# Performance work log

Hardware: AMD Instinct MI355X
Metric: run time of the kernel (lower is better)

The kernel has to match this reference:

```python
import jax, jax.numpy as jnp
import numpy as np

B, T, C, H = 8, 2048, 2048, 128  # batch, seq, n_embd, head_size


def setup_inputs() -> dict:
    key = jax.random.key(0)
    kx, kq, kk, kv = jax.random.split(key, 4)
    x = jax.random.normal(kx, (B, T, C), dtype=jnp.float32)
    # Linear(n_embd, head_size, bias=False); stored as [in, out] so x @ W matches x @ weight.T in torch
    Wq = jax.random.normal(kq, (C, H), dtype=jnp.float32) * 0.02
    Wk = jax.random.normal(kk, (C, H), dtype=jnp.float32) * 0.02
    Wv = jax.random.normal(kv, (C, H), dtype=jnp.float32) * 0.02
    return {"x": x, "Wq": Wq, "Wk": Wk, "Wv": Wv}


def reference(x, Wq, Wk, Wv):
    # Single-head scaled dot-product attention (mask=False path of the module)
    q = jnp.einsum("btc,ch->bth", x, Wq)  # [B,T,H]
    k = jnp.einsum("btc,ch->bth", x, Wk)
    v = jnp.einsum("btc,ch->bth", x, Wv)
    scale = k.shape[-1] ** -0.5
    wei = jnp.einsum("bqh,bkh->bqk", q, k) * scale  # [B,T,T]
    wei = jax.nn.softmax(wei, axis=-1)
    out = jnp.einsum("bqk,bkh->bqh", wei, v)  # [B,T,H]
    return out
```

## Files before the change

### kernel.cpp

```cpp
#include <hip/hip_runtime.h>
#include <hip/hip_bf16.h>

typedef __attribute__((ext_vector_type(8))) short short8;
typedef __attribute__((ext_vector_type(4))) float f32x4;

#define MFMA16(a, b, c) __builtin_amdgcn_mfma_f32_16x16x32_bf16((a), (b), (c), 0, 0, 0)

#define GLOAD_LDS16(gp, lp)                                                            \
    __builtin_amdgcn_global_load_lds(                                                  \
        (const __attribute__((address_space(1))) unsigned int*)(gp),                   \
        (__attribute__((address_space(3))) unsigned int*)(lp), 16, 0, 0)

__device__ __forceinline__ unsigned short f2bf(float f) {
    __hip_bfloat16 h = __float2bfloat16(f);
    return __builtin_bit_cast(unsigned short, h);
}

__device__ __forceinline__ short8 cvt8(f32x4 a, f32x4 b) {
    short8 r;
    r[0] = (short)f2bf(a[0]); r[1] = (short)f2bf(a[1]);
    r[2] = (short)f2bf(a[2]); r[3] = (short)f2bf(a[3]);
    r[4] = (short)f2bf(b[0]); r[5] = (short)f2bf(b[1]);
    r[6] = (short)f2bf(b[2]); r[7] = (short)f2bf(b[3]);
    return r;
}

__global__ __launch_bounds__(256) void wt_kernel(const float* __restrict__ Wq,
                                                 const float* __restrict__ Wk,
                                                 const float* __restrict__ Wv,
                                                 unsigned short* __restrict__ Wt) {
    __shared__ float T[64][65];
    const int j = blockIdx.z;
    const float* W = (j == 0) ? Wq : (j == 1) ? Wk : Wv;
    const int c0 = blockIdx.x * 64;
    const int h0 = blockIdx.y * 64;
    const int tid = threadIdx.x;

#pragma unroll
    for (int i = 0; i < 4; i++) {
        const int cc = tid + 256 * i;
        const int r = cc >> 4;
        const int q4 = (cc & 15) * 4;
        f32x4 vv = *(const f32x4*)(W + (size_t)(c0 + r) * 128 + h0 + q4);
        T[r][q4 + 0] = vv[0]; T[r][q4 + 1] = vv[1];
        T[r][q4 + 2] = vv[2]; T[r][q4 + 3] = vv[3];
    }
    __syncthreads();
#pragma unroll
    for (int i = 0; i < 2; i++) {
        const int oc = tid + 256 * i;
        const int hr = oc >> 3;
        const int c8 = (oc & 7) * 8;
        short8 r;
#pragma unroll
        for (int e = 0; e < 8; e++) r[e] = (short)f2bf(T[c8 + e][hr]);
        *(short8*)(Wt + (size_t)j * (128 * 2048) + (size_t)(h0 + hr) * 2048 + c0 + c8) = r;
    }
}

__global__ __launch_bounds__(256, 3) void qkv_gemm(const float* __restrict__ x,
                                                   const unsigned short* __restrict__ Wt,
                                                   unsigned short* __restrict__ qkv) {
    constexpr int LDA = 72;
    __shared__ __align__(16) unsigned short As[2][64 * LDA];
    __shared__ __align__(16) unsigned short Bs[2][128 * 64];

    const int tid = threadIdx.x;
    const int l = tid & 63;
    const int w = tid >> 6;
    const int wr = w >> 1, wc = w & 1;
    const int lrow = l & 15, g = l >> 4, lk = g * 8;

    const int p = blockIdx.x;
    const int wg = (p & 7) * 96 + (p >> 3);
    const int bn = wg % 3;
    const int bm = wg / 3;

    const float* xA = x + (size_t)bm * 64 * 2048;
    const unsigned short* Wb = Wt + (size_t)bn * (128 * 2048);
    unsigned short* outp = qkv + (size_t)bn * (16384 * 128);

    const int rowA = tid >> 2;
    const int quad = tid & 3;
    const float* srcA0 = xA + (size_t)rowA * 2048 + quad * 16;

    const int brow_base = (w << 5) + (l >> 3);
    const int bsw = ((l >> 3) & 7) << 4;
    const int bslot = (l & 7) << 4;
    const int bsrc_off = ((bslot ^ bsw) >> 1);

    const f32x4 fzero = {0.f, 0.f, 0.f, 0.f};
    f32x4 acc[2][4];
#pragma unroll
    for (int mt = 0; mt < 2; mt++)
#pragma unroll
        for (int nt = 0; nt < 4; nt++) acc[mt][nt] = fzero;

#pragma unroll
    for (int i = 0; i < 4; i++) {
        const int row = brow_base + (i << 3);
        GLOAD_LDS16(Wb + (size_t)row * 2048 + bsrc_off,
                    &Bs[0][(w << 11) + (i << 9)]);
    }
    {
        f32x4 a0 = *(const f32x4*)(srcA0);
        f32x4 a1 = *(const f32x4*)(srcA0 + 4);
        f32x4 a2 = *(const f32x4*)(srcA0 + 8);
        f32x4 a3 = *(const f32x4*)(srcA0 + 12);
        *(short8*)&As[0][rowA * LDA + quad * 16] = cvt8(a0, a1);
        *(short8*)&As[0][rowA * LDA + quad * 16 + 8] = cvt8(a2, a3);
    }
    __syncthreads();

    int cur = 0;
    for (int kt = 0; kt < 32; kt++) {
        f32x4 a0, a1, a2, a3;
        if (kt < 31) {
#pragma unroll
            for (int i = 0; i < 4; i++) {
                const int row = brow_base + (i << 3);
                GLOAD_LDS16(Wb + (size_t)row * 2048 + (kt + 1) * 64 + bsrc_off,
                            &Bs[cur ^ 1][(w << 11) + (i << 9)]);
            }
            const float* sA = srcA0 + (kt + 1) * 64;
            a0 = *(const f32x4*)(sA);
            a1 = *(const f32x4*)(sA + 4);
            a2 = *(const f32x4*)(sA + 8);
            a3 = *(const f32x4*)(sA + 12);
        }

#pragma unroll
        for (int ks = 0; ks < 2; ks++) {
            short8 af[2], bfr[4];
#pragma unroll
            for (int mt = 0; mt < 2; mt++)
                af[mt] = *(const short8*)&As[cur][(wr * 32 + mt * 16 + lrow) * LDA + ks * 32 + lk];
#pragma unroll
            for (int nt = 0; nt < 4; nt++) {
                const int n = wc * 64 + nt * 16 + lrow;
                const int kbyte = (ks * 64 + g * 16) ^ ((n & 7) << 4);
                bfr[nt] = *(const short8*)&Bs[cur][n * 64 + (kbyte >> 1)];
            }
#pragma unroll
            for (int mt = 0; mt < 2; mt++)
#pragma unroll
                for (int nt = 0; nt < 4; nt++)
                    acc[mt][nt] = MFMA16(af[mt], bfr[nt], acc[mt][nt]);
        }

        if (kt < 31) {
            *(short8*)&As[cur ^ 1][rowA * LDA + quad * 16] = cvt8(a0, a1);
            *(short8*)&As[cur ^ 1][rowA * LDA + quad * 16 + 8] = cvt8(a2, a3);
        }
        __syncthreads();
        cur ^= 1;
    }

    const float scale = (bn == 0) ? 0.08838834764831845f : 1.0f;
#pragma unroll
    for (int mt = 0; mt < 2; mt++)
#pragma unroll
        for (int nt = 0; nt < 4; nt++)
#pragma unroll
            for (int r = 0; r < 4; r++) {
                const int row = bm * 64 + wr * 32 + mt * 16 + g * 4 + r;
                const int col = wc * 64 + nt * 16 + lrow;
                outp[(size_t)row * 128 + col] = f2bf(acc[mt][nt][r] * scale);
            }
}

template <bool SPLIT>
__global__ __launch_bounds__(256) void attn_kernel_t(const unsigned short* __restrict__ q,
                                                     const unsigned short* __restrict__ k,
                                                     const unsigned short* __restrict__ v,
                                                     float* __restrict__ Oout,
                                                     float* __restrict__ Ml) {
    constexpr int KS = 136;
    constexpr int VS = 88;
    constexpr int PS = 88;
    __shared__ __align__(16) unsigned short Ks[64 * KS];
    __shared__ __align__(16) unsigned short Vt[128 * VS];
    __shared__ __align__(16) unsigned short Psh[64 * PS];

    const int tid = threadIdx.x;
    const int l = tid & 63;
    const int w = tid >> 6;
    const int qt = blockIdx.x;
    const int b = blockIdx.y;
    const int s = SPLIT ? blockIdx.z : 0;
    const int kv_beg = SPLIT ? s * 11 : 0;
    const int kv_end = SPLIT ? ((s == 2) ? 32 : kv_beg + 11) : 32;
    const int lrow = l & 15, g = l >> 4, lk = g * 8;

    const size_t qbase = ((size_t)b * 2048 + qt * 64 + w * 16 + lrow) * 128;
    short8 qf[4];
#pragma unroll
    for (int ks = 0; ks < 4; ks++) qf[ks] = *(const short8*)(q + qbase + ks * 32 + lk);

    const f32x4 fzero = {0.f, 0.f, 0.f, 0.f};
    float m_r[4], l_r[4];
    f32x4 oacc[8];
#pragma unroll
    for (int r = 0; r < 4; r++) { m_r[r] = -1e30f; l_r[r] = 0.f; }
#pragma unroll
    for (int d = 0; d < 8; d++) oacc[d] = fzero;

    const int skey = tid & 63;
    const int sd = (tid >> 6) * 8;

    for (int kv = kv_beg; kv < kv_end; kv++) {
        __syncthreads();
        const size_t kvbase = ((size_t)b * 2048 + kv * 64 + skey) * 128;
#pragma unroll
        for (int jj = 0; jj < 4; jj++) {
            const int d0 = sd + jj * 32;
            short8 kvv = *(const short8*)(k + kvbase + d0);
            *(short8*)&Ks[skey * KS + d0] = kvv;
        }
#pragma unroll
        for (int jj = 0; jj < 4; jj++) {
            const int d0 = sd + jj * 32;
            short8 vv = *(const short8*)(v + kvbase + d0);
#pragma unroll
            for (int e = 0; e < 8; e++)
                Vt[(d0 + e) * VS + skey] = (unsigned short)vv[e];
        }
        __syncthreads();

        f32x4 sv[4];
#pragma unroll
        for (int nt = 0; nt < 4; nt++) sv[nt] = fzero;
#pragma unroll
        for (int ks = 0; ks < 4; ks++)
#pragma unroll
            for (int nt = 0; nt < 4; nt++) {
                short8 kf = *(const short8*)&Ks[(nt * 16 + lrow) * KS + ks * 32 + lk];
                sv[nt] = MFMA16(qf[ks], kf, sv[nt]);
            }

        float sf[4];
#pragma unroll
        for (int r = 0; r < 4; r++) {
            float tmax = fmaxf(fmaxf(sv[0][r], sv[1][r]), fmaxf(sv[2][r], sv[3][r]));
#pragma unroll
            for (int mk = 8; mk >= 1; mk >>= 1) tmax = fmaxf(tmax, __shfl_xor(tmax, mk));
            const float mnew = fmaxf(m_r[r], tmax);
            sf[r] = __expf(m_r[r] - mnew);
            m_r[r] = mnew;
            float psum = 0.f;
#pragma unroll
            for (int nt = 0; nt < 4; nt++) {
                const float pp = __expf(sv[nt][r] - mnew);
                sv[nt][r] = pp;
                psum += pp;
            }
#pragma unroll
            for (int mk = 8; mk >= 1; mk >>= 1) psum += __shfl_xor(psum, mk);
            l_r[r] = l_r[r] * sf[r] + psum;
        }
#pragma unroll
        for (int d = 0; d < 8; d++)
#pragma unroll
            for (int r = 0; r < 4; r++) oacc[d][r] *= sf[r];

#pragma unroll
        for (int nt = 0; nt < 4; nt++)
#pragma unroll
            for (int r = 0; r < 4; r++)
                Psh[(w * 16 + g * 4 + r) * PS + nt * 16 + lrow] = f2bf(sv[nt][r]);
        __syncthreads();

#pragma unroll
        for (int ks2 = 0; ks2 < 2; ks2++) {
            short8 pa = *(const short8*)&Psh[(w * 16 + lrow) * PS + ks2 * 32 + lk];
#pragma unroll
            for (int dt = 0; dt < 8; dt++) {
                short8 vbf = *(const short8*)&Vt[(dt * 16 + lrow) * VS + ks2 * 32 + lk];
                oacc[dt] = MFMA16(pa, vbf, oacc[dt]);
            }
        }
    }

#pragma unroll
    for (int r = 0; r < 4; r++) {
        const int rowi = b * 2048 + qt * 64 + w * 16 + g * 4 + r;
        if (SPLIT) {
            const size_t obase = ((size_t)s * 16384 + rowi) * 128;
#pragma unroll
            for (int dt = 0; dt < 8; dt++)
                Oout[obase + dt * 16 + lrow] = oacc[dt][r];
            if (lrow == 0) {
                const size_t mb = ((size_t)s * 16384 + rowi) * 2;
                Ml[mb] = m_r[r];
                Ml[mb + 1] = l_r[r];
            }
        } else {
            const float inv = 1.0f / l_r[r];
#pragma unroll
            for (int dt = 0; dt < 8; dt++)
                Oout[(size_t)rowi * 128 + dt * 16 + lrow] = oacc[dt][r] * inv;
        }
    }
}

__global__ __launch_bounds__(256) void attn_merge(const float* __restrict__ Oacc,
                                                  const float* __restrict__ Ml,
                                                  float* __restrict__ out) {
    const int row = blockIdx.x * 2 + (threadIdx.x >> 7);
    const int c = threadIdx.x & 127;
    const float m0 = Ml[(size_t)(0 * 16384 + row) * 2], l0 = Ml[(size_t)(0 * 16384 + row) * 2 + 1];
    const float m1 = Ml[(size_t)(1 * 16384 + row) * 2], l1 = Ml[(size_t)(1 * 16384 + row) * 2 + 1];
    const float m2 = Ml[(size_t)(2 * 16384 + row) * 2], l2 = Ml[(size_t)(2 * 16384 + row) * 2 + 1];
    const float M = fmaxf(m0, fmaxf(m1, m2));
    const float w0 = __expf(m0 - M), w1 = __expf(m1 - M), w2 = __expf(m2 - M);
    const float D = w0 * l0 + w1 * l1 + w2 * l2;
    const float o = w0 * Oacc[(size_t)(0 * 16384 + row) * 128 + c] +
                    w1 * Oacc[(size_t)(1 * 16384 + row) * 128 + c] +
                    w2 * Oacc[(size_t)(2 * 16384 + row) * 128 + c];
    out[(size_t)row * 128 + c] = o / D;
}

extern "C" void kernel_launch(void* const* d_in, const int* in_sizes, int n_in,
                              void* d_out, int out_size, void* d_ws, size_t ws_size,
                              hipStream_t stream) {
    const float* x  = (const float*)d_in[0];
    const float* Wq = (const float*)d_in[1];
    const float* Wk = (const float*)d_in[2];
    const float* Wv = (const float*)d_in[3];
    float* out = (float*)d_out;

    unsigned short* ws = (unsigned short*)d_ws;
    unsigned short* qb = ws;
    unsigned short* kb = qb + (size_t)16384 * 128;
    unsigned short* vb = kb + (size_t)16384 * 128;
    unsigned short* Wt = vb + (size_t)16384 * 128;
    float* Oacc = (float*)(Wt + (size_t)3 * 128 * 2048);
    float* Ml = Oacc + (size_t)3 * 16384 * 128;
    const size_t ws_need = (size_t)((char*)(Ml + (size_t)3 * 16384 * 2) - (char*)d_ws);

    hipLaunchKernelGGL(wt_kernel, dim3(32, 2, 3), dim3(256), 0, stream, Wq, Wk, Wv, Wt);
    hipLaunchKernelGGL(qkv_gemm, dim3(768), dim3(256), 0, stream, x, Wt, qb);
    if (ws_size >= ws_need) {
        hipLaunchKernelGGL((attn_kernel_t<true>), dim3(32, 8, 3), dim3(256), 0, stream,
                           qb, kb, vb, Oacc, Ml);
        hipLaunchKernelGGL(attn_merge, dim3(8192), dim3(256), 0, stream, Oacc, Ml, out);
    } else {
        hipLaunchKernelGGL((attn_kernel_t<false>), dim3(32, 8), dim3(256), 0, stream,
                           qb, kb, vb, out, (float*)nullptr);
    }
}
```

Measured before the change: 293.0 us.

## Deepen QKV GEMM prefetch and pre-transpose V for register-prefetched split attention

```diff
diff --git a/kernel.cpp b/kernel.cpp
--- a/kernel.cpp
+++ b/kernel.cpp
@@ -61,8 +61,7 @@
 __global__ __launch_bounds__(256, 3) void qkv_gemm(const float* __restrict__ x,
                                                    const unsigned short* __restrict__ Wt,
                                                    unsigned short* __restrict__ qkv) {
-    constexpr int LDA = 72;
-    __shared__ __align__(16) unsigned short As[2][64 * LDA];
+    __shared__ __align__(16) unsigned short As[2][64 * 72];
     __shared__ __align__(16) unsigned short Bs[2][128 * 64];
 
     const int tid = threadIdx.x;
@@ -96,65 +95,88 @@
 #pragma unroll
         for (int nt = 0; nt < 4; nt++) acc[mt][nt] = fzero;
 
-#pragma unroll
-    for (int i = 0; i < 4; i++) {
-        const int row = brow_base + (i << 3);
-        GLOAD_LDS16(Wb + (size_t)row * 2048 + bsrc_off,
-                    &Bs[0][(w << 11) + (i << 9)]);
-    }
+    f32x4 pA[4], pB[4];
+
+#define QKV_COMPUTE(CUR)                                                               \
+    {                                                                                  \
+        _Pragma("unroll")                                                              \
+        for (int ks = 0; ks < 2; ks++) {                                               \
+            short8 af[2], bfr[4];                                                      \
+            _Pragma("unroll")                                                          \
+            for (int mt = 0; mt < 2; mt++)                                             \
+                af[mt] = *(const short8*)&As[CUR][(wr * 32 + mt * 16 + lrow) * 72 +    \
+                                                  ks * 32 + lk];                       \
+            _Pragma("unroll")                                                          \
+            for (int nt = 0; nt < 4; nt++) {                                           \
+                const int n = wc * 64 + nt * 16 + lrow;                                \
+                const int kbyte = (ks * 64 + g * 16) ^ ((n & 7) << 4);                 \
+                bfr[nt] = *(const short8*)&Bs[CUR][n * 64 + (kbyte >> 1)];             \
+            }                                                                          \
+            _Pragma("unroll")                                                          \
+            for (int mt = 0; mt < 2; mt++)                                             \
+                _Pragma("unroll")                                                      \
+                for (int nt = 0; nt < 4; nt++)                                         \
+                    acc[mt][nt] = MFMA16(af[mt], bfr[nt], acc[mt][nt]);                \
+        }                                                                              \
+    }
+
+#define QKV_ITER(KT, CUR, ARR, ISS, WAITSTR, DOISS)                                    \
+    {                                                                                  \
+        _Pragma("unroll")                                                              \
+        for (int i = 0; i < 4; i++) {                                                  \
+            const int row = brow_base + (i << 3);                                      \
+            GLOAD_LDS16(Wb + (size_t)row * 2048 + ((KT) + 1) * 64 + bsrc_off,          \
+                        &Bs[(CUR) ^ 1][(w << 11) + (i << 9)]);                         \
+        }                                                                              \
+        __builtin_amdgcn_sched_barrier(0);                                             \
+        if (DOISS) {                                                                   \
+            const float* sA = srcA0 + ((KT) + 2) * 64;                                 \
+            ISS[0] = *(const f32x4*)(sA);     ISS[1] = *(const f32x4*)(sA + 4);        \
+            ISS[2] = *(const f32x4*)(sA + 8); ISS[3] = *(const f32x4*)(sA + 12);       \
+        }                                                                              \
+        QKV_COMPUTE(CUR);                                                              \
+        *(short8*)&As[(CUR) ^ 1][rowA * 72 + quad * 16]     = cvt8(ARR[0], ARR[1]);    \
+        *(short8*)&As[(CUR) ^ 1][rowA * 72 + quad * 16 + 8] = cvt8(ARR[2], ARR[3]);    \
+        asm volatile(WAITSTR ::: "memory");                                            \
+        asm volatile("s_waitcnt lgkmcnt(0)" ::: "memory");                             \
+        __builtin_amdgcn_sched_barrier(0);                                             \
+        __builtin_amdgcn_s_barrier();                                                  \
+        __builtin_amdgcn_sched_barrier(0);                                             \
+    }
+
     {
         f32x4 a0 = *(const f32x4*)(srcA0);
         f32x4 a1 = *(const f32x4*)(srcA0 + 4);
         f32x4 a2 = *(const f32x4*)(srcA0 + 8);
         f32x4 a3 = *(const f32x4*)(srcA0 + 12);
-        *(short8*)&As[0][rowA * LDA + quad * 16] = cvt8(a0, a1);
-        *(short8*)&As[0][rowA * LDA + quad * 16 + 8] = cvt8(a2, a3);
-    }
-    __syncthreads();
-
-    int cur = 0;
-    for (int kt = 0; kt < 32; kt++) {
-        f32x4 a0, a1, a2, a3;
-        if (kt < 31) {
-#pragma unroll
-            for (int i = 0; i < 4; i++) {
-                const int row = brow_base + (i << 3);
-                GLOAD_LDS16(Wb + (size_t)row * 2048 + (kt + 1) * 64 + bsrc_off,
-                            &Bs[cur ^ 1][(w << 11) + (i << 9)]);
-            }
-            const float* sA = srcA0 + (kt + 1) * 64;
-            a0 = *(const f32x4*)(sA);
-            a1 = *(const f32x4*)(sA + 4);
-            a2 = *(const f32x4*)(sA + 8);
-            a3 = *(const f32x4*)(sA + 12);
-        }
-
-#pragma unroll
-        for (int ks = 0; ks < 2; ks++) {
-            short8 af[2], bfr[4];
-#pragma unroll
-            for (int mt = 0; mt < 2; mt++)
-                af[mt] = *(const short8*)&As[cur][(wr * 32 + mt * 16 + lrow) * LDA + ks * 32 + lk];
-#pragma unroll
-            for (int nt = 0; nt < 4; nt++) {
-                const int n = wc * 64 + nt * 16 + lrow;
-                const int kbyte = (ks * 64 + g * 16) ^ ((n & 7) << 4);
-                bfr[nt] = *(const short8*)&Bs[cur][n * 64 + (kbyte >> 1)];
-            }
-#pragma unroll
-            for (int mt = 0; mt < 2; mt++)
-#pragma unroll
-                for (int nt = 0; nt < 4; nt++)
-                    acc[mt][nt] = MFMA16(af[mt], bfr[nt], acc[mt][nt]);
-        }
-
-        if (kt < 31) {
-            *(short8*)&As[cur ^ 1][rowA * LDA + quad * 16] = cvt8(a0, a1);
-            *(short8*)&As[cur ^ 1][rowA * LDA + quad * 16 + 8] = cvt8(a2, a3);
-        }
-        __syncthreads();
-        cur ^= 1;
-    }
+        *(short8*)&As[0][rowA * 72 + quad * 16] = cvt8(a0, a1);
+        *(short8*)&As[0][rowA * 72 + quad * 16 + 8] = cvt8(a2, a3);
+#pragma unroll
+        for (int i = 0; i < 4; i++) {
+            const int row = brow_base + (i << 3);
+            GLOAD_LDS16(Wb + (size_t)row * 2048 + bsrc_off,
+                        &Bs[0][(w << 11) + (i << 9)]);
+        }
+        __builtin_amdgcn_sched_barrier(0);
+        const float* sA = srcA0 + 64;
+        pA[0] = *(const f32x4*)(sA);     pA[1] = *(const f32x4*)(sA + 4);
+        pA[2] = *(const f32x4*)(sA + 8); pA[3] = *(const f32x4*)(sA + 12);
+        asm volatile("s_waitcnt vmcnt(4)" ::: "memory");
+        asm volatile("s_waitcnt lgkmcnt(0)" ::: "memory");
+        __builtin_amdgcn_sched_barrier(0);
+        __builtin_amdgcn_s_barrier();
+        __builtin_amdgcn_sched_barrier(0);
+    }
+
+    for (int kt = 0; kt < 30; kt += 2) {
+        QKV_ITER(kt, 0, pA, pB, "s_waitcnt vmcnt(4)", true);
+        QKV_ITER(kt + 1, 1, pB, pA, "s_waitcnt vmcnt(4)", true);
+    }
+    QKV_ITER(30, 0, pA, pB, "s_waitcnt vmcnt(0)", false);
+    QKV_COMPUTE(1);
+
+#undef QKV_ITER
+#undef QKV_COMPUTE
 
     const float scale = (bn == 0) ? 0.08838834764831845f : 1.0f;
 #pragma unroll
@@ -169,12 +191,187 @@
             }
 }
 
-template <bool SPLIT>
-__global__ __launch_bounds__(256) void attn_kernel_t(const unsigned short* __restrict__ q,
+__global__ __launch_bounds__(256) void vt_kernel(const unsigned short* __restrict__ v,
+                                                 unsigned short* __restrict__ vT) {
+    __shared__ unsigned short T[64][72];
+    const int b = blockIdx.z;
+    const int t0 = blockIdx.x * 64;
+    const int h0 = blockIdx.y * 64;
+    const int tid = threadIdx.x;
+
+#pragma unroll
+    for (int i = 0; i < 2; i++) {
+        const int c = tid + 256 * i;
+        const int tr = c >> 3;
+        const int hc = (c & 7) * 8;
+        *(short8*)&T[tr][hc] =
+            *(const short8*)(v + ((size_t)(b * 2048 + t0 + tr)) * 128 + h0 + hc);
+    }
+    __syncthreads();
+#pragma unroll
+    for (int i = 0; i < 2; i++) {
+        const int c = tid + 256 * i;
+        const int hr = c >> 3;
+        const int tc = (c & 7) * 8;
+        short8 o;
+#pragma unroll
+        for (int e = 0; e < 8; e++) o[e] = (short)T[tc + e][hr];
+        *(short8*)(vT + ((size_t)(b * 128 + h0 + hr)) * 2048 + t0 + tc) = o;
+    }
+}
+
+__global__ __launch_bounds__(256, 3) void attn_split(const unsigned short* __restrict__ q,
                                                      const unsigned short* __restrict__ k,
-                                                     const unsigned short* __restrict__ v,
+                                                     const unsigned short* __restrict__ vT,
                                                      float* __restrict__ Oout,
                                                      float* __restrict__ Ml) {
+    constexpr int KS = 136;
+    constexpr int VS = 72;
+    constexpr int PS = 88;
+    __shared__ __align__(16) unsigned short Ks[64 * KS];
+    __shared__ __align__(16) unsigned short Vt[128 * VS];
+    __shared__ __align__(16) unsigned short Psh[64 * PS];
+
+    const int tid = threadIdx.x;
+    const int l = tid & 63;
+    const int w = tid >> 6;
+    const int qt = blockIdx.x;
+    const int b = blockIdx.y;
+    const int s = blockIdx.z;
+    const int kv_beg = s * 11;
+    const int kv_end = (s == 2) ? 32 : kv_beg + 11;
+    const int lrow = l & 15, g = l >> 4, lk = g * 8;
+
+    const size_t qbase = ((size_t)b * 2048 + qt * 64 + w * 16 + lrow) * 128;
+    short8 qf[4];
+#pragma unroll
+    for (int ks = 0; ks < 4; ks++) qf[ks] = *(const short8*)(q + qbase + ks * 32 + lk);
+
+    const f32x4 fzero = {0.f, 0.f, 0.f, 0.f};
+    float m_r[4], l_r[4];
+    f32x4 oacc[8];
+#pragma unroll
+    for (int r = 0; r < 4; r++) { m_r[r] = -1e30f; l_r[r] = 0.f; }
+#pragma unroll
+    for (int d = 0; d < 8; d++) oacc[d] = fzero;
+
+    const int skey = tid & 63;
+    const int sd = (tid >> 6) * 8;
+    const int vd = tid >> 1;
+    const int vh = tid & 1;
+    const unsigned short* vrow = vT + ((size_t)(b * 128 + vd)) * 2048;
+
+    short8 kr[4], vr[4];
+    {
+        const size_t kvbase = ((size_t)b * 2048 + kv_beg * 64 + skey) * 128;
+        const unsigned short* vsrc = vrow + kv_beg * 64 + vh * 32;
+#pragma unroll
+        for (int jj = 0; jj < 4; jj++) {
+            kr[jj] = *(const short8*)(k + kvbase + sd + jj * 32);
+            vr[jj] = *(const short8*)(vsrc + jj * 8);
+        }
+    }
+#pragma unroll
+    for (int jj = 0; jj < 4; jj++) {
+        *(short8*)&Ks[skey * KS + sd + jj * 32] = kr[jj];
+        *(short8*)&Vt[vd * VS + vh * 32 + jj * 8] = vr[jj];
+    }
+    __syncthreads();
+
+    for (int kv = kv_beg; kv < kv_end; kv++) {
+        const bool has_next = (kv + 1 < kv_end);
+        if (has_next) {
+            const size_t kvbase = ((size_t)b * 2048 + (kv + 1) * 64 + skey) * 128;
+            const unsigned short* vsrc = vrow + (kv + 1) * 64 + vh * 32;
+#pragma unroll
+            for (int jj = 0; jj < 4; jj++) {
+                kr[jj] = *(const short8*)(k + kvbase + sd + jj * 32);
+                vr[jj] = *(const short8*)(vsrc + jj * 8);
+            }
+        }
+
+        f32x4 sv[4];
+#pragma unroll
+        for (int nt = 0; nt < 4; nt++) sv[nt] = fzero;
+#pragma unroll
+        for (int ks = 0; ks < 4; ks++)
+#pragma unroll
+            for (int nt = 0; nt < 4; nt++) {
+                short8 kf = *(const short8*)&Ks[(nt * 16 + lrow) * KS + ks * 32 + lk];
+                sv[nt] = MFMA16(qf[ks], kf, sv[nt]);
+            }
+
+        float sf[4];
+#pragma unroll
+        for (int r = 0; r < 4; r++) {
+            float tmax = fmaxf(fmaxf(sv[0][r], sv[1][r]), fmaxf(sv[2][r], sv[3][r]));
+#pragma unroll
+            for (int mk = 8; mk >= 1; mk >>= 1) tmax = fmaxf(tmax, __shfl_xor(tmax, mk));
+            const float mnew = fmaxf(m_r[r], tmax);
+            sf[r] = __expf(m_r[r] - mnew);
+            m_r[r] = mnew;
+            float psum = 0.f;
+#pragma unroll
+            for (int nt = 0; nt < 4; nt++) {
+                const float pp = __expf(sv[nt][r] - mnew);
+                sv[nt][r] = pp;
+                psum += pp;
+            }
+#pragma unroll
+            for (int mk = 8; mk >= 1; mk >>= 1) psum += __shfl_xor(psum, mk);
+            l_r[r] = l_r[r] * sf[r] + psum;
+        }
+#pragma unroll
+        for (int d = 0; d < 8; d++)
+#pragma unroll
+            for (int r = 0; r < 4; r++) oacc[d][r] *= sf[r];
+
+#pragma unroll
+        for (int nt = 0; nt < 4; nt++)
+#pragma unroll
+            for (int r = 0; r < 4; r++)
+                Psh[(w * 16 + g * 4 + r) * PS + nt * 16 + lrow] = f2bf(sv[nt][r]);
+
+#pragma unroll
+        for (int ks2 = 0; ks2 < 2; ks2++) {
+            short8 pa = *(const short8*)&Psh[(w * 16 + lrow) * PS + ks2 * 32 + lk];
+#pragma unroll
+            for (int dt = 0; dt < 8; dt++) {
+                short8 vbf = *(const short8*)&Vt[(dt * 16 + lrow) * VS + ks2 * 32 + lk];
+                oacc[dt] = MFMA16(pa, vbf, oacc[dt]);
+            }
+        }
+
+        __syncthreads();
+        if (has_next) {
+#pragma unroll
+            for (int jj = 0; jj < 4; jj++) {
+                *(short8*)&Ks[skey * KS + sd + jj * 32] = kr[jj];
+                *(short8*)&Vt[vd * VS + vh * 32 + jj * 8] = vr[jj];
+            }
+        }
+        __syncthreads();
+    }
+
+#pragma unroll
+    for (int r = 0; r < 4; r++) {
+        const int rowi = b * 2048 + qt * 64 + w * 16 + g * 4 + r;
+        const size_t obase = ((size_t)s * 16384 + rowi) * 128;
+#pragma unroll
+        for (int dt = 0; dt < 8; dt++)
+            Oout[obase + dt * 16 + lrow] = oacc[dt][r];
+        if (lrow == 0) {
+            const size_t mb = ((size_t)s * 16384 + rowi) * 2;
+            Ml[mb] = m_r[r];
+            Ml[mb + 1] = l_r[r];
+        }
+    }
+}
+
+__global__ __launch_bounds__(256) void attn_single(const unsigned short* __restrict__ q,
+                                                   const unsigned short* __restrict__ k,
+                                                   const unsigned short* __restrict__ v,
+                                                   float* __restrict__ out) {
     constexpr int KS = 136;
     constexpr int VS = 88;
     constexpr int PS = 88;
@@ -187,9 +384,6 @@
     const int w = tid >> 6;
     const int qt = blockIdx.x;
     const int b = blockIdx.y;
-    const int s = SPLIT ? blockIdx.z : 0;
-    const int kv_beg = SPLIT ? s * 11 : 0;
-    const int kv_end = SPLIT ? ((s == 2) ? 32 : kv_beg + 11) : 32;
     const int lrow = l & 15, g = l >> 4, lk = g * 8;
 
     const size_t qbase = ((size_t)b * 2048 + qt * 64 + w * 16 + lrow) * 128;
@@ -208,22 +402,18 @@
     const int skey = tid & 63;
     const int sd = (tid >> 6) * 8;
 
-    for (int kv = kv_beg; kv < kv_end; kv++) {
+    for (int kv = 0; kv < 32; kv++) {
         __syncthreads();
         const size_t kvbase = ((size_t)b * 2048 + kv * 64 + skey) * 128;
 #pragma unroll
-        for (int jj = 0; jj < 4; jj++) {
-            const int d0 = sd + jj * 32;
-            short8 kvv = *(const short8*)(k + kvbase + d0);
-            *(short8*)&Ks[skey * KS + d0] = kvv;
-        }
+        for (int jj = 0; jj < 4; jj++)
+            *(short8*)&Ks[skey * KS + sd + jj * 32] = *(const short8*)(k + kvbase + sd + jj * 32);
 #pragma unroll
         for (int jj = 0; jj < 4; jj++) {
             const int d0 = sd + jj * 32;
             short8 vv = *(const short8*)(v + kvbase + d0);
 #pragma unroll
-            for (int e = 0; e < 8; e++)
-                Vt[(d0 + e) * VS + skey] = (unsigned short)vv[e];
+            for (int e = 0; e < 8; e++) Vt[(d0 + e) * VS + skey] = (unsigned short)vv[e];
         }
         __syncthreads();
 
@@ -284,22 +474,10 @@
 #pragma unroll
     for (int r = 0; r < 4; r++) {
         const int rowi = b * 2048 + qt * 64 + w * 16 + g * 4 + r;
-        if (SPLIT) {
-            const size_t obase = ((size_t)s * 16384 + rowi) * 128;
-#pragma unroll
-            for (int dt = 0; dt < 8; dt++)
-                Oout[obase + dt * 16 + lrow] = oacc[dt][r];
-            if (lrow == 0) {
-                const size_t mb = ((size_t)s * 16384 + rowi) * 2;
-                Ml[mb] = m_r[r];
-                Ml[mb + 1] = l_r[r];
-            }
-        } else {
-            const float inv = 1.0f / l_r[r];
-#pragma unroll
-            for (int dt = 0; dt < 8; dt++)
-                Oout[(size_t)rowi * 128 + dt * 16 + lrow] = oacc[dt][r] * inv;
-        }
+        const float inv = 1.0f / l_r[r];
+#pragma unroll
+        for (int dt = 0; dt < 8; dt++)
+            out[(size_t)rowi * 128 + dt * 16 + lrow] = oacc[dt][r] * inv;
     }
 }
 
@@ -334,18 +512,20 @@
     unsigned short* kb = qb + (size_t)16384 * 128;
     unsigned short* vb = kb + (size_t)16384 * 128;
     unsigned short* Wt = vb + (size_t)16384 * 128;
-    float* Oacc = (float*)(Wt + (size_t)3 * 128 * 2048);
+    unsigned short* vtb = Wt + (size_t)3 * 128 * 2048;
+    float* Oacc = (float*)(vtb + (size_t)8 * 128 * 2048);
     float* Ml = Oacc + (size_t)3 * 16384 * 128;
     const size_t ws_need = (size_t)((char*)(Ml + (size_t)3 * 16384 * 2) - (char*)d_ws);
 
     hipLaunchKernelGGL(wt_kernel, dim3(32, 2, 3), dim3(256), 0, stream, Wq, Wk, Wv, Wt);
     hipLaunchKernelGGL(qkv_gemm, dim3(768), dim3(256), 0, stream, x, Wt, qb);
     if (ws_size >= ws_need) {
-        hipLaunchKernelGGL((attn_kernel_t<true>), dim3(32, 8, 3), dim3(256), 0, stream,
-                           qb, kb, vb, Oacc, Ml);
+        hipLaunchKernelGGL(vt_kernel, dim3(32, 2, 8), dim3(256), 0, stream, vb, vtb);
+        hipLaunchKernelGGL(attn_split, dim3(32, 8, 3), dim3(256), 0, stream,
+                           qb, kb, vtb, Oacc, Ml);
         hipLaunchKernelGGL(attn_merge, dim3(8192), dim3(256), 0, stream, Oacc, Ml, out);
     } else {
-        hipLaunchKernelGGL((attn_kernel_t<false>), dim3(32, 8), dim3(256), 0, stream,
-                           qb, kb, vb, out, (float*)nullptr);
-    }
-}
+        hipLaunchKernelGGL(attn_single, dim3(32, 8), dim3(256), 0, stream,
+                           qb, kb, vb, out);
+    }
+}
```

Result: no change. 293.5 us (+0.2%).
